# Performance work log

Hardware: AMD Instinct MI355X
Metric: run time of the kernel (lower is better)

Reference implementation:

```python
import jax, jax.numpy as jnp
from jax import lax
import numpy as np

DIVISOR = 2.0  # init kwarg 'divisor'


def setup_inputs() -> dict:
    key = jax.random.key(0)
    k1, k2, k3, k4 = jax.random.split(key, 4)
    x = jax.random.normal(k1, (8, 32, 32, 64, 64), dtype=jnp.float32)        # N,C_in,D,H,W
    conv_weight = jax.random.normal(k2, (64, 32, 3, 3, 3), dtype=jnp.float32)  # O,I,kD,kH,kW
    conv_bias = jax.random.normal(k3, (64,), dtype=jnp.float32)
    bias = jax.random.normal(k4, (64, 1, 1, 1), dtype=jnp.float32)           # post bias (per out-channel)
    return {"x": x, "conv_weight": conv_weight, "conv_bias": conv_bias, "bias": bias}


def reference(x, conv_weight, conv_bias, bias):
    # Valid 3D conv, stride 1 (matches the CUDA kernel's sliding window)
    y = lax.conv_general_dilated(
        x, conv_weight,
        window_strides=(1, 1, 1), padding='VALID',
        dimension_numbers=('NCDHW', 'OIDHW', 'NCDHW'))
    # (conv + conv_bias) / divisor + post_bias, then sum over out-channels
    y = (y + conv_bias[None, :, None, None, None]) * (1.0 / DIVISOR) \
        + bias.reshape(1, -1, 1, 1, 1)
    return jnp.sum(y, axis=1)  # (N, D_out, H_out, W_out)
```

## Files before the change

kernel.cpp:

```cpp
#include <hip/hip_runtime.h>


#define XD 32
#define XH 64
#define XW 64
#define DOUT 30
#define HOUT 62
#define WOUT 62
#define CH_STRIDE (XD * XH * XW)

__device__ __forceinline__ float nextlane(float v) {
  return __int_as_float(
      __builtin_amdgcn_mov_dpp(__float_as_int(v), 0x101, 0xF, 0xF, true));
}

__global__ __launch_bounds__(256, 4)
void conv3d_chansum_reg(const float* __restrict__ x,
                        const float* __restrict__ cw,
                        const float* __restrict__ cb,
                        const float* __restrict__ pb,
                        float* __restrict__ out) {
  __shared__ float wl[1537];

  const int tid  = threadIdx.x;
  const int wid  = tid >> 6;
  const int lane = tid & 63;

  const int bid = blockIdx.x;
  const int swz = (bid & 7) * 128 + (bid >> 3);

  const int wslab = swz * 4 + wid;
  const int n  = wslab >> 9;
  const int d  = (wslab >> 4) & 31;
  const int h0 = (wslab & 15) * 4;

  const int s  = lane & 15;
  const int ht = lane >> 4;
  const bool alive = d < DOUT;

  if (tid < 216) {
    const float4* cw4 = (const float4*)(cw + 4 * tid);
    float4 sum = {0.f, 0.f, 0.f, 0.f};
#pragma unroll 8
    for (int o = 0; o < 64; ++o) {
      float4 v = cw4[o * 216];
      sum.x += v.x; sum.y += v.y; sum.z += v.z; sum.w += v.w;
    }
    float vs[4] = {sum.x, sum.y, sum.z, sum.w};
#pragma unroll
    for (int q = 0; q < 4; ++q) {
      int e  = 4 * tid + q;
      int i  = e / 27;
      int r  = e - i * 27;
      int kd = r / 9;
      int t  = r - kd * 9;
      wl[i * 48 + kd * 16 + t] = 0.5f * vs[q];
    }
  }
  if (tid < 64) {
    float v = 0.5f * cb[tid] + pb[tid];
#pragma unroll
    for (int off = 32; off > 0; off >>= 1) v += __shfl_xor(v, off, 64);
    if (tid == 0) wl[1536] = v;
  }
  __syncthreads();
  if (!alive) return;

  const float* xn = x + (size_t)n * (32u * CH_STRIDE);

  int soff[9];
#pragma unroll
  for (int kd = 0; kd < 3; ++kd)
#pragma unroll
    for (int kh = 0; kh < 3; ++kh) {
      int rc = min(h0 + ht + kh, XH - 1);
      soff[kd * 3 + kh] = (d + kd) * (XH * XW) + rc * XW + 4 * s;
    }

  float acc[4] = {0.f, 0.f, 0.f, 0.f};

#pragma unroll 1
  for (int ch = 0; ch < 32; ++ch) {
    const float* xnc = xn + (size_t)ch * CH_STRIDE;

    float4 a[9];
#pragma unroll
    for (int i = 0; i < 9; ++i)
      a[i] = *(const float4*)(xnc + soff[i]);

    const float* wrow = &wl[ch * 48];
#pragma unroll
    for (int kd = 0; kd < 3; ++kd) {
      float4 w0 = *(const float4*)(wrow + kd * 16);
      float4 w1 = *(const float4*)(wrow + kd * 16 + 4);
      float  w8 = wrow[kd * 16 + 8];
      float wt[9] = {w0.x, w0.y, w0.z, w0.w, w1.x, w1.y, w1.z, w1.w, w8};
#pragma unroll
      for (int kh = 0; kh < 3; ++kh) {
        float4 av = a[kd * 3 + kh];
        float x4v = nextlane(av.x);
        float x5v = nextlane(av.y);
        float xv[6] = {av.x, av.y, av.z, av.w, x4v, x5v};
#pragma unroll
        for (int j = 0; j < 4; ++j)
          acc[j] = fmaf(xv[j],     wt[kh * 3 + 0],
                   fmaf(xv[j + 1], wt[kh * 3 + 1],
                   fmaf(xv[j + 2], wt[kh * 3 + 2], acc[j])));
      }
    }
  }

  const float Cc = wl[1536];
  const int h = h0 + ht;
  if (h < HOUT) {
    float* op = out + (((size_t)n * DOUT + d) * HOUT + h) * WOUT + 4 * s;
    const int nw = min(4, WOUT - 4 * s);
    float2 v0 = {acc[0] + Cc, acc[1] + Cc};
    *(float2*)op = v0;
    if (nw == 4) {
      float2 v1 = {acc[2] + Cc, acc[3] + Cc};
      *(float2*)(op + 2) = v1;
    }
  }
}

extern "C" void kernel_launch(void* const* d_in, const int* in_sizes, int n_in,
                              void* d_out, int out_size, void* d_ws, size_t ws_size,
                              hipStream_t stream) {
  const float* x  = (const float*)d_in[0];
  const float* cw = (const float*)d_in[1];
  const float* cb = (const float*)d_in[2];
  const float* pb = (const float*)d_in[3];
  float* out = (float*)d_out;

  conv3d_chansum_reg<<<dim3(1024), 256, 0, stream>>>(x, cw, cb, pb, out);
}
```

Before: 244.9 us.

## Double-buffer per-channel input loads with sched barriers to overlap memory and FMA

Restructures the channel loop into a two-stage software pipeline: the next channel's nine float4 loads are issued into a second register set before computing the current channel. Scheduling barriers keep the compiler from sinking those loads past the compute. It also unrolls the weight-summing loop further. The aim is to hide global load latency behind FMAs, at the cost of about 36 extra VGPRs, which may hurt occupancy under launch_bounds(256,4). It also adds one redundant load of channel 31 on the final iteration.

```diff
diff --git a/kernel.cpp b/kernel.cpp
--- a/kernel.cpp
+++ b/kernel.cpp
@@ -13,6 +13,48 @@
   return __int_as_float(
       __builtin_amdgcn_mov_dpp(__float_as_int(v), 0x101, 0xF, 0xF, true));
 }
+
+#define ROWFMA(av, t0, t1, t2)                                        \
+  do {                                                                \
+    const float4 _av = (av);                                          \
+    const float _x4 = nextlane(_av.x);                                \
+    const float _x5 = nextlane(_av.y);                                \
+    acc0 = fmaf(_av.x, (t0), fmaf(_av.y, (t1), fmaf(_av.z, (t2), acc0))); \
+    acc1 = fmaf(_av.y, (t0), fmaf(_av.z, (t1), fmaf(_av.w, (t2), acc1))); \
+    acc2 = fmaf(_av.z, (t0), fmaf(_av.w, (t1), fmaf(_x4,  (t2), acc2))); \
+    acc3 = fmaf(_av.w, (t0), fmaf(_x4,  (t1), fmaf(_x5,  (t2), acc3))); \
+  } while (0)
+
+#define LOAD_SET(p, v0, v1, v2, v3, v4, v5, v6, v7, v8)  \
+  do {                                                   \
+    v0 = *(const float4*)((p) + o0);                     \
+    v1 = *(const float4*)((p) + o1);                     \
+    v2 = *(const float4*)((p) + o2);                     \
+    v3 = *(const float4*)((p) + o3);                     \
+    v4 = *(const float4*)((p) + o4);                     \
+    v5 = *(const float4*)((p) + o5);                     \
+    v6 = *(const float4*)((p) + o6);                     \
+    v7 = *(const float4*)((p) + o7);                     \
+    v8 = *(const float4*)((p) + o8);                     \
+  } while (0)
+
+#define KD_BLOCK(wrow, kdoff, v0, v1, v2)                 \
+  do {                                                    \
+    const float4 _wA = *(const float4*)((wrow) + (kdoff));     \
+    const float4 _wB = *(const float4*)((wrow) + (kdoff) + 4); \
+    const float  _w8 = (wrow)[(kdoff) + 8];               \
+    ROWFMA(v0, _wA.x, _wA.y, _wA.z);                      \
+    ROWFMA(v1, _wA.w, _wB.x, _wB.y);                      \
+    ROWFMA(v2, _wB.z, _wB.w, _w8);                        \
+  } while (0)
+
+#define COMPUTE_SET(ch, v0, v1, v2, v3, v4, v5, v6, v7, v8) \
+  do {                                                      \
+    const float* _wrow = &wl[(ch) * 48];                    \
+    KD_BLOCK(_wrow, 0,  v0, v1, v2);                        \
+    KD_BLOCK(_wrow, 16, v3, v4, v5);                        \
+    KD_BLOCK(_wrow, 32, v6, v7, v8);                        \
+  } while (0)
 
 __global__ __launch_bounds__(256, 4)
 void conv3d_chansum_reg(const float* __restrict__ x,
@@ -41,7 +83,7 @@
   if (tid < 216) {
     const float4* cw4 = (const float4*)(cw + 4 * tid);
     float4 sum = {0.f, 0.f, 0.f, 0.f};
-#pragma unroll 8
+#pragma unroll 16
     for (int o = 0; o < 64; ++o) {
       float4 v = cw4[o * 216];
       sum.x += v.x; sum.y += v.y; sum.z += v.z; sum.w += v.w;
@@ -68,46 +110,31 @@
 
   const float* xn = x + (size_t)n * (32u * CH_STRIDE);
 
-  int soff[9];
-#pragma unroll
-  for (int kd = 0; kd < 3; ++kd)
-#pragma unroll
-    for (int kh = 0; kh < 3; ++kh) {
-      int rc = min(h0 + ht + kh, XH - 1);
-      soff[kd * 3 + kh] = (d + kd) * (XH * XW) + rc * XW + 4 * s;
-    }
+#define OFFS(kd, kh) \
+  ((d + (kd)) * (XH * XW) + min(h0 + ht + (kh), XH - 1) * XW + 4 * s)
+  const int o0 = OFFS(0, 0), o1 = OFFS(0, 1), o2 = OFFS(0, 2);
+  const int o3 = OFFS(1, 0), o4 = OFFS(1, 1), o5 = OFFS(1, 2);
+  const int o6 = OFFS(2, 0), o7 = OFFS(2, 1), o8 = OFFS(2, 2);
+#undef OFFS
 
-  float acc[4] = {0.f, 0.f, 0.f, 0.f};
+  float acc0 = 0.f, acc1 = 0.f, acc2 = 0.f, acc3 = 0.f;
+
+  float4 a0, a1, a2, a3, a4, a5, a6, a7, a8;
+  float4 b0, b1, b2, b3, b4, b5, b6, b7, b8;
+
+  LOAD_SET(xn, a0, a1, a2, a3, a4, a5, a6, a7, a8);
 
 #pragma unroll 1
-  for (int ch = 0; ch < 32; ++ch) {
-    const float* xnc = xn + (size_t)ch * CH_STRIDE;
+  for (int ch = 0; ch < 32; ch += 2) {
+    const float* x1 = xn + (size_t)(ch + 1) * CH_STRIDE;
+    LOAD_SET(x1, b0, b1, b2, b3, b4, b5, b6, b7, b8);
+    __builtin_amdgcn_sched_barrier(0);
+    COMPUTE_SET(ch, a0, a1, a2, a3, a4, a5, a6, a7, a8);
 
-    float4 a[9];
-#pragma unroll
-    for (int i = 0; i < 9; ++i)
-      a[i] = *(const float4*)(xnc + soff[i]);
-
-    const float* wrow = &wl[ch * 48];
-#pragma unroll
-    for (int kd = 0; kd < 3; ++kd) {
-      float4 w0 = *(const float4*)(wrow + kd * 16);
-      float4 w1 = *(const float4*)(wrow + kd * 16 + 4);
-      float  w8 = wrow[kd * 16 + 8];
-      float wt[9] = {w0.x, w0.y, w0.z, w0.w, w1.x, w1.y, w1.z, w1.w, w8};
-#pragma unroll
-      for (int kh = 0; kh < 3; ++kh) {
-        float4 av = a[kd * 3 + kh];
-        float x4v = nextlane(av.x);
-        float x5v = nextlane(av.y);
-        float xv[6] = {av.x, av.y, av.z, av.w, x4v, x5v};
-#pragma unroll
-        for (int j = 0; j < 4; ++j)
-          acc[j] = fmaf(xv[j],     wt[kh * 3 + 0],
-                   fmaf(xv[j + 1], wt[kh * 3 + 1],
-                   fmaf(xv[j + 2], wt[kh * 3 + 2], acc[j])));
-      }
-    }
+    const float* x2 = xn + (size_t)min(ch + 2, 31) * CH_STRIDE;
+    LOAD_SET(x2, a0, a1, a2, a3, a4, a5, a6, a7, a8);
+    __builtin_amdgcn_sched_barrier(0);
+    COMPUTE_SET(ch + 1, b0, b1, b2, b3, b4, b5, b6, b7, b8);
   }
 
   const float Cc = wl[1536];
@@ -115,10 +142,10 @@
   if (h < HOUT) {
     float* op = out + (((size_t)n * DOUT + d) * HOUT + h) * WOUT + 4 * s;
     const int nw = min(4, WOUT - 4 * s);
-    float2 v0 = {acc[0] + Cc, acc[1] + Cc};
+    float2 v0 = {acc0 + Cc, acc1 + Cc};
     *(float2*)op = v0;
     if (nw == 4) {
-      float2 v1 = {acc[2] + Cc, acc[3] + Cc};
+      float2 v1 = {acc2 + Cc, acc3 + Cc};
       *(float2*)(op + 2) = v1;
     }
   }
```

Result: slower. 557.1 us (+127.5%).
